# Optimization experiments

Hardware: AMD Instinct MI355X
Metric: run time of the kernel (lower is better)

## Reference

```python
import jax, jax.numpy as jnp
import numpy as np

N_USER = 100000
N_ITEM = 100000
SUPP = 10000
B = 1024
L = 50
S = 256
H = 4
E = 64
HID = 64


def setup_inputs() -> dict:
    key = jax.random.key(0)
    ks = jax.random.split(key, 32)
    f32 = jnp.float32
    inp = {}
    # forward int args
    inp["x"] = jax.random.randint(ks[0], (B, 2), 0, N_USER)
    inp["src_his"] = jax.random.randint(ks[1], (B, L), 0, N_ITEM)
    inp["src_hl"] = jax.random.randint(ks[2], (B,), 0, L)
    inp["tgt_his"] = jax.random.randint(ks[3], (B, L), 0, N_ITEM)
    inp["tgt_hl"] = jax.random.randint(ks[4], (B,), 0, L)
    # precomputed neighbor sampling: [2 get_user_emb calls, H heads, B, S]
    inp["sample_idx"] = jax.random.randint(ks[5], (2, H, B, S), 0, SUPP)
    inp["supp_users"] = jax.random.randint(ks[6], (SUPP,), 0, N_USER)
    # embedding tables (xavier-ish small scale)
    inp["src_user_emb"] = jax.random.normal(ks[7], (N_USER, E), f32) * 0.1
    inp["src_item_emb"] = jax.random.normal(ks[8], (N_ITEM, E), f32) * 0.1
    inp["tgt_user_emb"] = jax.random.normal(ks[9], (N_USER, E), f32) * 0.1
    inp["tgt_item_emb"] = jax.random.normal(ks[10], (N_ITEM, E), f32) * 0.1
    # attention / aggregation weights, stored [in, out]
    s = 1.0 / np.sqrt(E)
    inp["W_att_w"] = jax.random.normal(ks[11], (E, E), f32) * s
    inp["W_att_b"] = jnp.full((E,), 0.1, f32)
    inp["W_agg_w"] = jax.random.normal(ks[12], (E, E), f32) * s
    # per-head GAT projections, batched over heads
    inp["Wq"] = jax.random.normal(ks[13], (H, E, E), f32) * s
    inp["Wk"] = jax.random.normal(ks[14], (H, E, E), f32) * s
    inp["Wv"] = jax.random.normal(ks[15], (H, E, E), f32) * s
    inp["W_out"] = jax.random.normal(ks[16], (H * E, E), f32) * (1.0 / np.sqrt(H * E))
    # scoring MLP
    inp["l1_w"] = jax.random.normal(ks[17], (2 * E, HID), f32) * (1.0 / np.sqrt(2 * E))
    inp["l1_b"] = jnp.full((HID,), 0.1, f32)
    inp["l2_w"] = jax.random.normal(ks[18], (HID, E), f32) * (1.0 / np.sqrt(HID))
    inp["l2_b"] = jnp.full((E,), 0.1, f32)
    inp["l3_w"] = jax.random.normal(ks[19], (E, 1), f32) * s
    inp["l3_b"] = jnp.full((1,), 0.1, f32)
    return inp


def reference(x, src_his, src_hl, tgt_his, tgt_hl, sample_idx, supp_users,
              src_user_emb, src_item_emb, tgt_user_emb, tgt_item_emb,
              W_att_w, W_att_b, W_agg_w, Wq, Wk, Wv, W_out,
              l1_w, l1_b, l2_w, l2_b, l3_w, l3_b):
    user_id = x[:, 0]
    item_id = x[:, 1]

    def user_fea_encode(his, hl, user_table):
        # NOTE: original always gathers from src_model.item_embedding (even for tgt)
        Lh = his.shape[1]
        valid = jnp.arange(Lh)[None, :] < hl[:, None]          # [B,L]
        hist = src_item_emb[his] * valid[..., None]             # [B,L,E], padded rows zeroed
        u = user_table[user_id]                                 # [B,E]
        keyt = jnp.tanh(hist @ W_att_w + W_att_b)               # [B,L,E]
        pad = hist.sum(-1) == 0                                 # [B,L]
        att = jnp.einsum('ble,be->bl', keyt, u)
        # faithful masked_softmax: masked scores set to 0 BEFORE exp (exp(0)=1 still contributes)
        att = jnp.where(pad, 0.0, att)
        e = jnp.exp(att)
        att = e / (jnp.sum(e, axis=1, keepdims=True) + 1e-12)
        out = jnp.einsum('bl,ble->be', att, hist)
        return out @ W_agg_w                                    # W_agg has no bias

    def get_user_emb(fea, idx):
        # idx: [H,B,S] indices into supp_users; all heads batched in one einsum chain
        neigh = tgt_user_emb[supp_users[idx]]                   # [H,B,S,E]
        q = jnp.einsum('be,heo->hbo', fea, Wq)                  # [H,B,O]
        k = jnp.einsum('hbse,heo->hbso', neigh, Wk)             # [H,B,S,O]
        attn = jax.nn.softmax(jnp.einsum('hbo,hbso->hbs', q, k), axis=-1)
        ctx = jnp.einsum('hbs,hbso->hbo', attn, k)              # weighted sum over neighbors
        g = jnp.einsum('hbo,hop->hbp', ctx, Wv)                 # [H,B,O]
        g = jnp.transpose(g, (1, 0, 2)).reshape(fea.shape[0], -1)  # concat heads -> [B,H*O]
        return g @ W_out

    user_src_fea = user_fea_encode(src_his, src_hl, src_user_emb)
    user_emb = get_user_emb(user_src_fea, sample_idx[0])
    item_emb = tgt_item_emb[item_id]
    user_tgt_fea = user_fea_encode(tgt_his, tgt_hl, tgt_user_emb)
    hybrid_tgt_emb = get_user_emb(user_tgt_fea, sample_idx[1])

    x_t = jnp.concatenate([hybrid_tgt_emb, item_emb], axis=1)
    x1_t = jnp.tanh(x_t @ l1_w + l1_b)
    x2_t = jnp.tanh(x1_t @ l2_w + l2_b)
    x3_t = (x2_t @ l3_w + l3_b).reshape(-1)

    output = jnp.sum(user_emb * item_emb, axis=1)
    out_emb_s = user_emb * item_emb
    # (output, output_t, out_emb_s, out_emb_t); train=False branch (sim/domain heads are None)
    return (output, x3_t, out_emb_s, x2_t)
```

## Files before the change

kernel.cpp:

```cpp
#include <hip/hip_runtime.h>

constexpr int B    = 1024;
constexpr int L    = 50;
constexpr int S    = 256;
constexpr int H    = 4;
constexpr int E    = 64;
constexpr int HID  = 64;
constexpr int SUPP = 10000;

__device__ __forceinline__ float lanebc(float v, int l) {
    return __int_as_float(__builtin_amdgcn_readlane(__float_as_int(v), l));
}

__device__ __forceinline__ float bcdot64(float v, const float* w) {
    float a0 = 0.0f, a1 = 0.0f, a2 = 0.0f, a3 = 0.0f;
#pragma unroll
    for (int i = 0; i < E; i += 4) {
        a0 += lanebc(v, i)     * w[i];
        a1 += lanebc(v, i + 1) * w[i + 1];
        a2 += lanebc(v, i + 2) * w[i + 2];
        a3 += lanebc(v, i + 3) * w[i + 3];
    }
    return (a0 + a1) + (a2 + a3);
}

__global__ __launch_bounds__(256) void pre_kernel(
    const int* __restrict__ x,
    const int* __restrict__ src_his,
    const int* __restrict__ src_hl,
    const int* __restrict__ tgt_his,
    const int* __restrict__ tgt_hl,
    const float* __restrict__ item_emb,
    const float* __restrict__ src_user_emb,
    const float* __restrict__ tgt_user_emb,
    const int* __restrict__ supp_users,
    const float* __restrict__ W_att_w,
    const float* __restrict__ W_att_b,
    const float* __restrict__ W_agg_w,
    const float* __restrict__ Wq,
    const float* __restrict__ Wk,
    float* __restrict__ qout,
    float* __restrict__ K_supp)
{
    const int tid  = threadIdx.x;
    const int lane = tid & 63;
    const int wave = tid >> 6;

    if (blockIdx.y == 2) {
        const int h = wave;
        float wcol[E];
#pragma unroll
        for (int i = 0; i < E; i++) wcol[i] = Wk[h * E * E + i * E + lane];

#pragma unroll 2
        for (int j = blockIdx.x; j < SUPP; j += gridDim.x) {
            const int u = supp_users[j];
            const float ev = tgt_user_emb[(size_t)u * E + lane];
            K_supp[((size_t)h * SUPP + j) * E + lane] = bcdot64(ev, wcol);
        }
        return;
    }

    __shared__ float sHist[L * E];
    __shared__ float sAtt[L];
    __shared__ float sPart[4][E];
    __shared__ float sOut[E];

    const int b    = blockIdx.x;
    const int call = blockIdx.y;

    const int* his = call ? tgt_his : src_his;
    const int* hl  = call ? tgt_hl  : src_hl;
    const float* user_table = call ? tgt_user_emb : src_user_emb;

    float wcol[E];
#pragma unroll
    for (int i = 0; i < E; i++) wcol[i] = W_att_w[i * E + lane];

    const int uid    = x[2 * b];
    const float uv   = user_table[(size_t)uid * E + lane];
    const float bias = W_att_b[lane];
    const int hlen   = hl[b];

    {
        int l = wave;
        float hv = 0.0f;
        if (l < L) {
            const int it = his[b * L + l];
            hv = (l < hlen) ? item_emb[(size_t)it * E + lane] : 0.0f;
        }
        while (l < L) {
            const int lnext = l + 4;
            float hv_next = 0.0f;
            if (lnext < L) {
                const int it = his[b * L + lnext];
                hv_next = (lnext < hlen) ? item_emb[(size_t)it * E + lane] : 0.0f;
            }
            sHist[l * E + lane] = hv;
            const float a = bias + bcdot64(hv, wcol);
            float part = tanhf(a) * uv;
            float hsum = hv;
#pragma unroll
            for (int off = 32; off; off >>= 1) {
                part += __shfl_xor(part, off);
                hsum += __shfl_xor(hsum, off);
            }
            if (lane == 0) sAtt[l] = (hsum == 0.0f) ? 0.0f : part;
            hv = hv_next;
            l  = lnext;
        }
    }
    __syncthreads();

    if (wave == 0) {
        float v = (lane < L) ? expf(sAtt[lane]) : 0.0f;
        float s = v;
#pragma unroll
        for (int off = 32; off; off >>= 1) s += __shfl_xor(s, off);
        const float denom = s + 1e-12f;
        if (lane < L) sAtt[lane] = v / denom;
    }
    __syncthreads();

    {
        float c0 = 0.0f, c1 = 0.0f;
        for (int l = wave; l < L; l += 8) c0 += sAtt[l] * sHist[l * E + lane];
        for (int l = wave + 4; l < L; l += 8) c1 += sAtt[l] * sHist[l * E + lane];
        sPart[wave][lane] = c0 + c1;
    }
    __syncthreads();
    if (tid < E) sOut[tid] = sPart[0][tid] + sPart[1][tid] + sPart[2][tid] + sPart[3][tid];
    __syncthreads();

    {
        float g0 = 0.0f, g1 = 0.0f, g2 = 0.0f, g3 = 0.0f;
#pragma unroll
        for (int k = 0; k < 16; k += 4) {
            const int i = wave * 16 + k;
            g0 += sOut[i]     * W_agg_w[i * E + lane];
            g1 += sOut[i + 1] * W_agg_w[(i + 1) * E + lane];
            g2 += sOut[i + 2] * W_agg_w[(i + 2) * E + lane];
            g3 += sOut[i + 3] * W_agg_w[(i + 3) * E + lane];
        }
        sPart[wave][lane] = (g0 + g1) + (g2 + g3);
    }
    __syncthreads();

    const float fval = sPart[0][lane] + sPart[1][lane] + sPart[2][lane] + sPart[3][lane];
    const float* Wqh = Wq + wave * E * E;
    float q0 = 0.0f, q1 = 0.0f, q2 = 0.0f, q3 = 0.0f;
#pragma unroll
    for (int i = 0; i < E; i += 4) {
        q0 += lanebc(fval, i)     * Wqh[i * E + lane];
        q1 += lanebc(fval, i + 1) * Wqh[(i + 1) * E + lane];
        q2 += lanebc(fval, i + 2) * Wqh[(i + 2) * E + lane];
        q3 += lanebc(fval, i + 3) * Wqh[(i + 3) * E + lane];
    }
    qout[(((call * H) + wave) * B + b) * E + lane] = (q0 + q1) + (q2 + q3);
}

__global__ __launch_bounds__(256) void attn_kernel(
    const int* __restrict__ sample_idx,
    const float* __restrict__ K_supp,
    const float* __restrict__ qarr,
    const float* __restrict__ Wv,
    float* __restrict__ gout)
{
    __shared__ float sRed[8];
    __shared__ float sCtx[4][E];
    __shared__ float sC[E];
    __shared__ float sG[4][E];

    const int b    = blockIdx.x;
    const int h    = blockIdx.y;
    const int call = blockIdx.z;
    const int tid  = threadIdx.x;
    const int lane = tid & 63;
    const int wave = tid >> 6;
    const int u    = lane & 15;
    const int rsub = lane >> 4;
    const int s0   = wave * 64;

    const int* idx = sample_idx + (((call * H) + h) * B + b) * S;
    const float* Kh = K_supp + (size_t)h * SUPP * E;
    const float4 qu = *(const float4*)(qarr + ((size_t)(((call * H) + h) * B + b)) * E + 4 * u);

    float4 kreg[16];
    float mylogit = 0.0f;
#pragma unroll
    for (int i = 0; i < 16; i++) {
        const int j = idx[s0 + 4 * i + rsub];
        kreg[i] = *(const float4*)(Kh + (size_t)j * E + 4 * u);
        float part = kreg[i].x * qu.x + kreg[i].y * qu.y
                   + kreg[i].z * qu.z + kreg[i].w * qu.w;
#pragma unroll
        for (int off = 1; off < 16; off <<= 1) part += __shfl_xor(part, off);
        mylogit = (u == i) ? part : mylogit;
    }

    float m = mylogit;
#pragma unroll
    for (int off = 32; off; off >>= 1) m = fmaxf(m, __shfl_xor(m, off));
    if (lane == 0) sRed[wave] = m;
    __syncthreads();
    const float mx = fmaxf(fmaxf(sRed[0], sRed[1]), fmaxf(sRed[2], sRed[3]));
    const float ex = expf(mylogit - mx);
    float sm = ex;
#pragma unroll
    for (int off = 32; off; off >>= 1) sm += __shfl_xor(sm, off);
    if (lane == 0) sRed[4 + wave] = sm;
    __syncthreads();
    const float denom = sRed[4] + sRed[5] + sRed[6] + sRed[7];
    const float pval = ex / denom;

    float4 cacc = make_float4(0.0f, 0.0f, 0.0f, 0.0f);
#pragma unroll
    for (int i = 0; i < 16; i++) {
        const float p = __shfl(pval, (lane & 48) + i);
        cacc.x += p * kreg[i].x;
        cacc.y += p * kreg[i].y;
        cacc.z += p * kreg[i].z;
        cacc.w += p * kreg[i].w;
    }
#pragma unroll
    for (int off = 16; off <= 32; off <<= 1) {
        cacc.x += __shfl_xor(cacc.x, off);
        cacc.y += __shfl_xor(cacc.y, off);
        cacc.z += __shfl_xor(cacc.z, off);
        cacc.w += __shfl_xor(cacc.w, off);
    }
    if (lane < 16) *(float4*)(&sCtx[wave][u * 4]) = cacc;
    __syncthreads();
    if (wave == 0) {
        sC[lane] = sCtx[0][lane] + sCtx[1][lane] + sCtx[2][lane] + sCtx[3][lane];
    }
    __syncthreads();

    const float* Wvh = Wv + h * E * E;
    float g0 = 0.0f, g1 = 0.0f, g2 = 0.0f, g3 = 0.0f;
#pragma unroll
    for (int k = 0; k < 16; k += 4) {
        const int c = wave * 16 + k;
        g0 += sC[c]     * Wvh[c * E + lane];
        g1 += sC[c + 1] * Wvh[(c + 1) * E + lane];
        g2 += sC[c + 2] * Wvh[(c + 2) * E + lane];
        g3 += sC[c + 3] * Wvh[(c + 3) * E + lane];
    }
    sG[wave][lane] = (g0 + g1) + (g2 + g3);
    __syncthreads();
    if (wave == 0) {
        gout[((size_t)(call * B) + b) * (H * E) + h * E + lane] =
            sG[0][lane] + sG[1][lane] + sG[2][lane] + sG[3][lane];
    }
}

__global__ __launch_bounds__(256) void final_kernel(
    const int* __restrict__ x,
    const float* __restrict__ tgt_item_emb,
    const float* __restrict__ gsrc,
    const float* __restrict__ gtgt,
    const float* __restrict__ W_out,
    const float* __restrict__ l1_w,
    const float* __restrict__ l1_b,
    const float* __restrict__ l2_w,
    const float* __restrict__ l2_b,
    const float* __restrict__ l3_w,
    const float* __restrict__ l3_b,
    float* __restrict__ out)
{
    __shared__ float sPart[4][E];
    __shared__ float sHyb[E];
    __shared__ float sItem[E];
    __shared__ float sX1[HID];

    const int b    = blockIdx.x;
    const int tid  = threadIdx.x;
    const int lane = tid & 63;
    const int wave = tid >> 6;

    if (tid < E) {
        const int item = x[2 * b + 1];
        sItem[tid] = tgt_item_emb[(size_t)item * E + tid];
    }

    const float* grow = (wave < 2) ? (gsrc + (size_t)b * (H * E))
                                   : (gtgt + (size_t)b * (H * E));
    const int i0 = (wave & 1) * 128;
    float a0 = 0.0f, a1 = 0.0f, a2 = 0.0f, a3 = 0.0f;
    for (int i = i0; i < i0 + 128; i += 4) {
        a0 += grow[i]     * W_out[i * E + lane];
        a1 += grow[i + 1] * W_out[(i + 1) * E + lane];
        a2 += grow[i + 2] * W_out[(i + 2) * E + lane];
        a3 += grow[i + 3] * W_out[(i + 3) * E + lane];
    }
    sPart[wave][lane] = (a0 + a1) + (a2 + a3);
    __syncthreads();

    if (wave == 0) {
        const float ue = sPart[0][lane] + sPart[1][lane];
        const float prod = ue * sItem[lane];
        out[2 * B + b * E + lane] = prod;
        float s = prod;
#pragma unroll
        for (int off = 32; off; off >>= 1) s += __shfl_xor(s, off);
        if (lane == 0) out[b] = s;
    }
    if (wave == 1) {
        sHyb[lane] = sPart[2][lane] + sPart[3][lane];
    }
    __syncthreads();

    {
        float b0 = 0.0f, b1 = 0.0f, b2 = 0.0f, b3 = 0.0f;
#pragma unroll
        for (int k = 0; k < 32; k += 4) {
            const int i = wave * 32 + k;
            const float v0 = (i < 64)     ? sHyb[i]          : sItem[i - 64];
            const float v1 = (i + 1 < 64) ? sHyb[i + 1]      : sItem[i + 1 - 64];
            const float v2 = (i + 2 < 64) ? sHyb[i + 2]      : sItem[i + 2 - 64];
            const float v3 = (i + 3 < 64) ? sHyb[i + 3]      : sItem[i + 3 - 64];
            b0 += v0 * l1_w[i * HID + lane];
            b1 += v1 * l1_w[(i + 1) * HID + lane];
            b2 += v2 * l1_w[(i + 2) * HID + lane];
            b3 += v3 * l1_w[(i + 3) * HID + lane];
        }
        sPart[wave][lane] = (b0 + b1) + (b2 + b3);
    }
    __syncthreads();

    if (wave == 0) {
        const float a = l1_b[lane] + sPart[0][lane] + sPart[1][lane]
                      + sPart[2][lane] + sPart[3][lane];
        sX1[lane] = tanhf(a);
    }
    __syncthreads();

    {
        float c0 = 0.0f, c1 = 0.0f, c2 = 0.0f, c3 = 0.0f;
#pragma unroll
        for (int k = 0; k < 16; k += 4) {
            const int i = wave * 16 + k;
            c0 += sX1[i]     * l2_w[i * E + lane];
            c1 += sX1[i + 1] * l2_w[(i + 1) * E + lane];
            c2 += sX1[i + 2] * l2_w[(i + 2) * E + lane];
            c3 += sX1[i + 3] * l2_w[(i + 3) * E + lane];
        }
        sPart[wave][lane] = (c0 + c1) + (c2 + c3);
    }
    __syncthreads();

    if (wave == 0) {
        const float a = l2_b[lane] + sPart[0][lane] + sPart[1][lane]
                      + sPart[2][lane] + sPart[3][lane];
        const float x2 = tanhf(a);
        out[2 * B + B * E + b * E + lane] = x2;
        float p = x2 * l3_w[lane];
#pragma unroll
        for (int off = 32; off; off >>= 1) p += __shfl_xor(p, off);
        if (lane == 0) out[B + b] = p + l3_b[0];
    }
}

extern "C" void kernel_launch(void* const* d_in, const int* in_sizes, int n_in,
                              void* d_out, int out_size, void* d_ws, size_t ws_size,
                              hipStream_t stream) {
    const int*   x            = (const int*)d_in[0];
    const int*   src_his      = (const int*)d_in[1];
    const int*   src_hl       = (const int*)d_in[2];
    const int*   tgt_his      = (const int*)d_in[3];
    const int*   tgt_hl       = (const int*)d_in[4];
    const int*   sample_idx   = (const int*)d_in[5];
    const int*   supp_users   = (const int*)d_in[6];
    const float* src_user_emb = (const float*)d_in[7];
    const float* src_item_emb = (const float*)d_in[8];
    const float* tgt_user_emb = (const float*)d_in[9];
    const float* tgt_item_emb = (const float*)d_in[10];
    const float* W_att_w      = (const float*)d_in[11];
    const float* W_att_b      = (const float*)d_in[12];
    const float* W_agg_w      = (const float*)d_in[13];
    const float* Wq           = (const float*)d_in[14];
    const float* Wk           = (const float*)d_in[15];
    const float* Wv           = (const float*)d_in[16];
    const float* W_out        = (const float*)d_in[17];
    const float* l1_w         = (const float*)d_in[18];
    const float* l1_b         = (const float*)d_in[19];
    const float* l2_w         = (const float*)d_in[20];
    const float* l2_b         = (const float*)d_in[21];
    const float* l3_w         = (const float*)d_in[22];
    const float* l3_b         = (const float*)d_in[23];

    float* ws      = (float*)d_ws;
    float* qarr    = ws;
    float* K_supp  = qarr + 2 * H * B * E;
    float* garr    = K_supp + H * SUPP * E;
    float* out     = (float*)d_out;

    pre_kernel<<<dim3(B, 3), 256, 0, stream>>>(
        x, src_his, src_hl, tgt_his, tgt_hl, src_item_emb,
        src_user_emb, tgt_user_emb, supp_users,
        W_att_w, W_att_b, W_agg_w, Wq, Wk, qarr, K_supp);
    attn_kernel<<<dim3(B, H, 2), 256, 0, stream>>>(
        sample_idx, K_supp, qarr, Wv, garr);
    final_kernel<<<dim3(B), 256, 0, stream>>>(
        x, tgt_item_emb, garr, garr + B * H * E, W_out,
        l1_w, l1_b, l2_w, l2_b, l3_w, l3_b, out);
}
```

Measured before the change: 290.1 us.

## Batch history gathers into shared memory and flatten attention grid ordering

The pre-kernel now issues all item-embedding gathers for the history up front into shared memory, followed by a sync, rather than software-pipelining one row ahead. This exposes more memory-level parallelism. The attention kernel's 3D grid becomes a 1D grid with head and call as the fastest-varying indices, so blocks for the same batch row run together, which may improve cache locality for the q rows and sample indices. Several dot-product loops also drop from four to two accumulators, which shortens dependency chains less and may lower register pressure.

```diff
diff --git a/kernel.cpp b/kernel.cpp
--- a/kernel.cpp
+++ b/kernel.cpp
@@ -13,15 +13,13 @@
 }
 
 __device__ __forceinline__ float bcdot64(float v, const float* w) {
-    float a0 = 0.0f, a1 = 0.0f, a2 = 0.0f, a3 = 0.0f;
-#pragma unroll
-    for (int i = 0; i < E; i += 4) {
+    float a0 = 0.0f, a1 = 0.0f;
+#pragma unroll
+    for (int i = 0; i < E; i += 2) {
         a0 += lanebc(v, i)     * w[i];
         a1 += lanebc(v, i + 1) * w[i + 1];
-        a2 += lanebc(v, i + 2) * w[i + 2];
-        a3 += lanebc(v, i + 3) * w[i + 3];
-    }
-    return (a0 + a1) + (a2 + a3);
+    }
+    return a0 + a1;
 }
 
 __global__ __launch_bounds__(256) void pre_kernel(
@@ -82,33 +80,27 @@
     const float bias = W_att_b[lane];
     const int hlen   = hl[b];
 
-    {
-        int l = wave;
-        float hv = 0.0f;
+#pragma unroll
+    for (int i = 0; i < 13; i++) {
+        const int l = wave + 4 * i;
         if (l < L) {
             const int it = his[b * L + l];
-            hv = (l < hlen) ? item_emb[(size_t)it * E + lane] : 0.0f;
-        }
-        while (l < L) {
-            const int lnext = l + 4;
-            float hv_next = 0.0f;
-            if (lnext < L) {
-                const int it = his[b * L + lnext];
-                hv_next = (lnext < hlen) ? item_emb[(size_t)it * E + lane] : 0.0f;
-            }
-            sHist[l * E + lane] = hv;
-            const float a = bias + bcdot64(hv, wcol);
-            float part = tanhf(a) * uv;
-            float hsum = hv;
-#pragma unroll
-            for (int off = 32; off; off >>= 1) {
-                part += __shfl_xor(part, off);
-                hsum += __shfl_xor(hsum, off);
-            }
-            if (lane == 0) sAtt[l] = (hsum == 0.0f) ? 0.0f : part;
-            hv = hv_next;
-            l  = lnext;
-        }
+            sHist[l * E + lane] = (l < hlen) ? item_emb[(size_t)it * E + lane] : 0.0f;
+        }
+    }
+    __syncthreads();
+
+    for (int l = wave; l < L; l += 4) {
+        const float hv = sHist[l * E + lane];
+        const float a = bias + bcdot64(hv, wcol);
+        float part = tanhf(a) * uv;
+        float hsum = hv;
+#pragma unroll
+        for (int off = 32; off; off >>= 1) {
+            part += __shfl_xor(part, off);
+            hsum += __shfl_xor(hsum, off);
+        }
+        if (lane == 0) sAtt[l] = (hsum == 0.0f) ? 0.0f : part;
     }
     __syncthreads();
 
@@ -133,30 +125,26 @@
     __syncthreads();
 
     {
-        float g0 = 0.0f, g1 = 0.0f, g2 = 0.0f, g3 = 0.0f;
-#pragma unroll
-        for (int k = 0; k < 16; k += 4) {
+        float g0 = 0.0f, g1 = 0.0f;
+#pragma unroll
+        for (int k = 0; k < 16; k += 2) {
             const int i = wave * 16 + k;
             g0 += sOut[i]     * W_agg_w[i * E + lane];
             g1 += sOut[i + 1] * W_agg_w[(i + 1) * E + lane];
-            g2 += sOut[i + 2] * W_agg_w[(i + 2) * E + lane];
-            g3 += sOut[i + 3] * W_agg_w[(i + 3) * E + lane];
-        }
-        sPart[wave][lane] = (g0 + g1) + (g2 + g3);
+        }
+        sPart[wave][lane] = g0 + g1;
     }
     __syncthreads();
 
     const float fval = sPart[0][lane] + sPart[1][lane] + sPart[2][lane] + sPart[3][lane];
     const float* Wqh = Wq + wave * E * E;
-    float q0 = 0.0f, q1 = 0.0f, q2 = 0.0f, q3 = 0.0f;
-#pragma unroll
-    for (int i = 0; i < E; i += 4) {
+    float q0 = 0.0f, q1 = 0.0f;
+#pragma unroll
+    for (int i = 0; i < E; i += 2) {
         q0 += lanebc(fval, i)     * Wqh[i * E + lane];
         q1 += lanebc(fval, i + 1) * Wqh[(i + 1) * E + lane];
-        q2 += lanebc(fval, i + 2) * Wqh[(i + 2) * E + lane];
-        q3 += lanebc(fval, i + 3) * Wqh[(i + 3) * E + lane];
-    }
-    qout[(((call * H) + wave) * B + b) * E + lane] = (q0 + q1) + (q2 + q3);
+    }
+    qout[(((call * H) + wave) * B + b) * E + lane] = q0 + q1;
 }
 
 __global__ __launch_bounds__(256) void attn_kernel(
@@ -171,9 +159,10 @@
     __shared__ float sC[E];
     __shared__ float sG[4][E];
 
-    const int b    = blockIdx.x;
-    const int h    = blockIdx.y;
-    const int call = blockIdx.z;
+    const int bid  = blockIdx.x;
+    const int h    = bid & 3;
+    const int call = (bid >> 2) & 1;
+    const int b    = bid >> 3;
     const int tid  = threadIdx.x;
     const int lane = tid & 63;
     const int wave = tid >> 6;
@@ -237,16 +226,14 @@
     __syncthreads();
 
     const float* Wvh = Wv + h * E * E;
-    float g0 = 0.0f, g1 = 0.0f, g2 = 0.0f, g3 = 0.0f;
-#pragma unroll
-    for (int k = 0; k < 16; k += 4) {
+    float g0 = 0.0f, g1 = 0.0f;
+#pragma unroll
+    for (int k = 0; k < 16; k += 2) {
         const int c = wave * 16 + k;
         g0 += sC[c]     * Wvh[c * E + lane];
         g1 += sC[c + 1] * Wvh[(c + 1) * E + lane];
-        g2 += sC[c + 2] * Wvh[(c + 2) * E + lane];
-        g3 += sC[c + 3] * Wvh[(c + 3) * E + lane];
-    }
-    sG[wave][lane] = (g0 + g1) + (g2 + g3);
+    }
+    sG[wave][lane] = g0 + g1;
     __syncthreads();
     if (wave == 0) {
         gout[((size_t)(call * B) + b) * (H * E) + h * E + lane] =
@@ -399,7 +386,7 @@
         x, src_his, src_hl, tgt_his, tgt_hl, src_item_emb,
         src_user_emb, tgt_user_emb, supp_users,
         W_att_w, W_att_b, W_agg_w, Wq, Wk, qarr, K_supp);
-    attn_kernel<<<dim3(B, H, 2), 256, 0, stream>>>(
+    attn_kernel<<<dim3(B * H * 2), 256, 0, stream>>>(
         sample_idx, K_supp, qarr, Wv, garr);
     final_kernel<<<dim3(B), 256, 0, stream>>>(
         x, tgt_item_emb, garr, garr + B * H * E, W_out,
```

New measurement: 292.0 us. About the same (+0.7%).
